# Kernel optimization log

Hardware: AMD Instinct MI355X
Metric: run time of the kernel (lower is better)

## Reference

```python
import jax, jax.numpy as jnp
import numpy as np

EPS = 1e-8  # torch cosine_similarity default eps


def compute_similarity(x, k, dilation=1):
    # x: [B, C, H, W]; returns [B, k*k-1, H, W] cosine similarity of each
    # pixel's channel vector vs its k x k neighborhood (center excluded).
    B, C, H, W = x.shape
    pad = (k // 2) * dilation
    # im2col: [B, C*k*k, H, W], channels ordered (C, kh, kw)
    patches = jax.lax.conv_general_dilated_patches(
        x, (k, k), (1, 1), padding=[(pad, pad), (pad, pad)],
        rhs_dilation=(dilation, dilation))
    patches = patches.reshape(B, C, k * k, H, W)
    center = patches[:, :, k * k // 2]                      # [B, C, H, W]
    dot = jnp.einsum('bchw,bcphw->bphw', center, patches)   # [B, k*k, H, W]
    n_center = jnp.sqrt(jnp.sum(center * center, axis=1))   # [B, H, W]
    n_patch = jnp.sqrt(jnp.sum(patches * patches, axis=1))  # [B, k*k, H, W]
    sim = dot / jnp.maximum(n_center[:, None] * n_patch, EPS)
    # drop the center (self-similarity == 1)
    c = k * k // 2
    return jnp.concatenate([sim[:, :c], sim[:, c + 1:]], axis=1)


def setup_inputs() -> dict:
    key = jax.random.key(0)
    x = jax.random.normal(key, (2, 128, 96, 96), dtype=jnp.float32)
    return {
        'x': x,
        'edge_threshold1': jnp.float32(0.3),
        'edge_threshold2': jnp.float32(0.3),
    }


def reference(x, edge_threshold1, edge_threshold2):
    LARGE_K, SMALL_K, DIL = 9, 5, 1
    large_sim = compute_similarity(x, LARGE_K, DIL)            # [B, 80, H, W]
    large_mask = (large_sim < edge_threshold1).astype(jnp.float32)
    large_mask = jnp.sqrt(jnp.sum(large_mask * large_mask, axis=1, keepdims=True))  # L2 norm over offsets
    x_mask = large_mask * x + x
    small_sim = compute_similarity(x_mask, SMALL_K, DIL)       # [B, 24, H, W]
    small_mask = (small_sim < edge_threshold2).astype(jnp.float32)
    small_mask = jnp.sqrt(jnp.sum(small_mask * small_mask, axis=1, keepdims=True))
    edge_map = x * small_mask + x
    return edge_map
```

## Files before the change

### kernel.cpp

```cpp
#include <hip/hip_runtime.h>

#define BN   2
#define CN   128
#define HN   96
#define WN   96
#define HW   (HN * WN)
#define NPIX (BN * HW)
#define NP4  (NPIX / 4)
#define NMAP 13
#define EPSV 1e-8f

constexpr int ODY[12] = {0, 0, 1, 1, 1, 1, 1, 2, 2, 2, 2, 2};
constexpr int ODX[12] = {1, 2, -2, -1, 0, 1, 2, -2, -1, 0, 1, 2};

__global__ void __launch_bounds__(256) k_maps(const float* __restrict__ x,
                                              float* __restrict__ D) {
    const int tx = threadIdx.x;
    const int ty = threadIdx.y;
    int p4 = blockIdx.x * 8 + tx;
    int pix = p4 * 4;
    int b = pix / HW;
    int hw = pix - b * HW;
    int h = hw / WN;
    int w = hw - h * WN;
    const float* xb = x + ((size_t)b * CN + (size_t)ty * 4) * HW + h * WN + w;

    float acc[NMAP][4];
#pragma unroll
    for (int m = 0; m < NMAP; ++m)
#pragma unroll
        for (int i = 0; i < 4; ++i) acc[m][i] = 0.f;

#pragma unroll
    for (int cc = 0; cc < 4; ++cc) {
        const float* cp = xb + (size_t)cc * HW;
        float r[3][12];
#pragma unroll
        for (int ry = 0; ry < 3; ++ry) {
            float4 a0 = make_float4(0.f, 0.f, 0.f, 0.f);
            float4 a1 = make_float4(0.f, 0.f, 0.f, 0.f);
            float4 a2 = make_float4(0.f, 0.f, 0.f, 0.f);
            if (h + ry < HN) {
                const float* rp = cp + ry * WN;
                if (w > 0)       a0 = *(const float4*)(rp - 4);
                a1 = *(const float4*)(rp);
                if (w + 4 < WN)  a2 = *(const float4*)(rp + 4);
            }
            r[ry][0] = a0.x; r[ry][1] = a0.y; r[ry][2]  = a0.z; r[ry][3]  = a0.w;
            r[ry][4] = a1.x; r[ry][5] = a1.y; r[ry][6]  = a1.z; r[ry][7]  = a1.w;
            r[ry][8] = a2.x; r[ry][9] = a2.y; r[ry][10] = a2.z; r[ry][11] = a2.w;
        }
#pragma unroll
        for (int i = 0; i < 4; ++i) {
            float c = r[0][4 + i];
            acc[0][i] += c * c;
#pragma unroll
            for (int j = 0; j < 12; ++j)
                acc[j + 1][i] += c * r[ODY[j]][4 + i + ODX[j]];
        }
    }

    __shared__ float red[16][8][53];
#pragma unroll
    for (int s = 16; s >= 1; s >>= 1) {
        if (ty >= s && ty < 2 * s) {
#pragma unroll
            for (int m = 0; m < NMAP; ++m)
#pragma unroll
                for (int i = 0; i < 4; ++i)
                    red[ty - s][tx][m * 4 + i] = acc[m][i];
        }
        __syncthreads();
        if (ty < s) {
#pragma unroll
            for (int m = 0; m < NMAP; ++m)
#pragma unroll
                for (int i = 0; i < 4; ++i)
                    acc[m][i] += red[ty][tx][m * 4 + i];
        }
        __syncthreads();
    }

    if (ty == 0) {
#pragma unroll
        for (int m = 0; m < NMAP; ++m)
            *(float4*)(D + (size_t)m * NPIX + pix) =
                make_float4(acc[m][0], acc[m][1], acc[m][2], acc[m][3]);
    }
}

template<int CSPLIT>
__global__ void __launch_bounds__(64) k_maskapply(const float* __restrict__ x,
                                                  const float* __restrict__ D,
                                                  const float* __restrict__ thr2p,
                                                  float* __restrict__ out) {
    int p = blockIdx.x * blockDim.x + threadIdx.x;
    if (p >= NPIX) return;
    int cg = blockIdx.y;
    const float t2 = *thr2p;
    int b = p / HW;
    int hw = p - b * HW;
    int h = hw / WN, w = hw - h * WN;

    float nc = sqrtf(D[p]);
    int count = 0;
#pragma unroll
    for (int j = 0; j < 12; ++j) {
        const int dy = ODY[j], dx = ODX[j];
        const float* Dj = D + (size_t)(j + 1) * NPIX;
        {
            float sim = 0.f;
            if (h + dy < HN && w + dx >= 0 && w + dx < WN) {
                int q = p + dy * WN + dx;
                sim = Dj[p] / fmaxf(nc * sqrtf(D[q]), EPSV);
            }
            count += (sim < t2) ? 1 : 0;
        }
        {
            float sim = 0.f;
            if (h - dy >= 0 && w - dx >= 0 && w - dx < WN) {
                int q = p - (dy * WN + dx);
                sim = Dj[q] / fmaxf(nc * sqrtf(D[q]), EPSV);
            }
            count += (sim < t2) ? 1 : 0;
        }
    }
    float s = 1.f + sqrtf((float)count);

    constexpr int CG = CN / CSPLIT;
    const float* xp = x   + ((size_t)b * CN + (size_t)cg * CG) * HW + hw;
    float*       op = out + ((size_t)b * CN + (size_t)cg * CG) * HW + hw;
#pragma unroll 8
    for (int c = 0; c < CG; ++c)
        op[(size_t)c * HW] = xp[(size_t)c * HW] * s;
}

extern "C" void kernel_launch(void* const* d_in, const int* in_sizes, int n_in,
                              void* d_out, int out_size, void* d_ws, size_t ws_size,
                              hipStream_t stream) {
    const float* x    = (const float*)d_in[0];
    const float* thr2 = (const float*)d_in[2];
    float* out = (float*)d_out;

    float* D = (float*)d_ws;

    k_maps<<<dim3(NP4 / 8), dim3(8, 32), 0, stream>>>(x, D);
    k_maskapply<4><<<dim3(NPIX / 64, 4), 64, 0, stream>>>(x, D, thr2, out);
}
```

Measured before the change: 87.93 us.

## Trim neighbor row loads, vectorize shared reduction, widen channel split in mask kernel

In the map kernel, each channel row now loads only the two extra columns it needs on either side (float2) instead of full float4 neighbors. Row 0 skips the left load entirely. The shared-memory reduction stores and loads float4 values instead of scalars. The mask-apply kernel uses 8 channel groups instead of 4 and fully unrolls its channel loop, trading more launched blocks and recomputed masks for more parallelism. The intent is to cut load traffic and LDS instruction count.

Measured after the change: 87.42 us. About the same (-0.6%).

```diff
diff --git a/kernel.cpp b/kernel.cpp
--- a/kernel.cpp
+++ b/kernel.cpp
@@ -34,49 +34,57 @@
 #pragma unroll
     for (int cc = 0; cc < 4; ++cc) {
         const float* cp = xb + (size_t)cc * HW;
-        float r[3][12];
+        float r[3][8];
+        {
+            float4 a1 = *(const float4*)cp;
+            float2 hi = make_float2(0.f, 0.f);
+            if (w + 4 < WN) hi = *(const float2*)(cp + 4);
+            r[0][0] = 0.f;  r[0][1] = 0.f;
+            r[0][2] = a1.x; r[0][3] = a1.y; r[0][4] = a1.z; r[0][5] = a1.w;
+            r[0][6] = hi.x; r[0][7] = hi.y;
+        }
 #pragma unroll
-        for (int ry = 0; ry < 3; ++ry) {
-            float4 a0 = make_float4(0.f, 0.f, 0.f, 0.f);
+        for (int ry = 1; ry < 3; ++ry) {
+            float2 lo = make_float2(0.f, 0.f);
             float4 a1 = make_float4(0.f, 0.f, 0.f, 0.f);
-            float4 a2 = make_float4(0.f, 0.f, 0.f, 0.f);
+            float2 hi = make_float2(0.f, 0.f);
             if (h + ry < HN) {
                 const float* rp = cp + ry * WN;
-                if (w > 0)       a0 = *(const float4*)(rp - 4);
-                a1 = *(const float4*)(rp);
-                if (w + 4 < WN)  a2 = *(const float4*)(rp + 4);
+                if (w > 0)      lo = *(const float2*)(rp - 2);
+                a1 = *(const float4*)rp;
+                if (w + 4 < WN) hi = *(const float2*)(rp + 4);
             }
-            r[ry][0] = a0.x; r[ry][1] = a0.y; r[ry][2]  = a0.z; r[ry][3]  = a0.w;
-            r[ry][4] = a1.x; r[ry][5] = a1.y; r[ry][6]  = a1.z; r[ry][7]  = a1.w;
-            r[ry][8] = a2.x; r[ry][9] = a2.y; r[ry][10] = a2.z; r[ry][11] = a2.w;
+            r[ry][0] = lo.x; r[ry][1] = lo.y;
+            r[ry][2] = a1.x; r[ry][3] = a1.y; r[ry][4] = a1.z; r[ry][5] = a1.w;
+            r[ry][6] = hi.x; r[ry][7] = hi.y;
         }
 #pragma unroll
         for (int i = 0; i < 4; ++i) {
-            float c = r[0][4 + i];
+            float c = r[0][2 + i];
             acc[0][i] += c * c;
 #pragma unroll
             for (int j = 0; j < 12; ++j)
-                acc[j + 1][i] += c * r[ODY[j]][4 + i + ODX[j]];
+                acc[j + 1][i] += c * r[ODY[j]][2 + i + ODX[j]];
         }
     }
 
-    __shared__ float red[16][8][53];
+    __shared__ float4 red[16][8][17];
 #pragma unroll
     for (int s = 16; s >= 1; s >>= 1) {
         if (ty >= s && ty < 2 * s) {
 #pragma unroll
             for (int m = 0; m < NMAP; ++m)
-#pragma unroll
-                for (int i = 0; i < 4; ++i)
-                    red[ty - s][tx][m * 4 + i] = acc[m][i];
+                red[ty - s][tx][m] =
+                    make_float4(acc[m][0], acc[m][1], acc[m][2], acc[m][3]);
         }
         __syncthreads();
         if (ty < s) {
 #pragma unroll
-            for (int m = 0; m < NMAP; ++m)
-#pragma unroll
-                for (int i = 0; i < 4; ++i)
-                    acc[m][i] += red[ty][tx][m * 4 + i];
+            for (int m = 0; m < NMAP; ++m) {
+                float4 v = red[ty][tx][m];
+                acc[m][0] += v.x; acc[m][1] += v.y;
+                acc[m][2] += v.z; acc[m][3] += v.w;
+            }
         }
         __syncthreads();
     }
@@ -130,7 +138,7 @@
     constexpr int CG = CN / CSPLIT;
     const float* xp = x   + ((size_t)b * CN + (size_t)cg * CG) * HW + hw;
     float*       op = out + ((size_t)b * CN + (size_t)cg * CG) * HW + hw;
-#pragma unroll 8
+#pragma unroll
     for (int c = 0; c < CG; ++c)
         op[(size_t)c * HW] = xp[(size_t)c * HW] * s;
 }
@@ -145,5 +153,5 @@
     float* D = (float*)d_ws;
 
     k_maps<<<dim3(NP4 / 8), dim3(8, 32), 0, stream>>>(x, D);
-    k_maskapply<4><<<dim3(NPIX / 64, 4), 64, 0, stream>>>(x, D, thr2, out);
+    k_maskapply<8><<<dim3(NPIX / 64, 8), 64, 0, stream>>>(x, D, thr2, out);
 }
```
